# Optimization experiments

Hardware: AMD Instinct MI355X
Metric: run time of the kernel (lower is better)

The kernel has to match this reference:

```python
import jax, jax.numpy as jnp
import numpy as np

N, E = 20000, 320000
NF, EF = 4, 4
HID, HEADS, MODEL_HID = 128, 4, 128


def _p(key, shape, scale=0.1):
    return scale * jax.random.normal(key, shape, dtype=jnp.float32)


def setup_inputs() -> dict:
    key = jax.random.key(0)
    ks = jax.random.split(key, 32)
    x = jax.random.normal(ks[0], (N, NF), dtype=jnp.float32)
    src = jax.random.randint(ks[1], (E,), 0, N)
    off = jax.random.randint(ks[2], (E,), 1, N)
    dst = (src + off) % N  # no self-loops (PyG removes then re-adds them)
    edge_index = jnp.stack([src, dst]).astype(jnp.int64)
    edge_attr = jax.random.uniform(ks[3], (E, EF), dtype=jnp.float32)
    d = dict(x=x, edge_index=edge_index, edge_attr=edge_attr)
    # input_proj
    d['Wp'] = _p(ks[4], (NF, HID)); d['bp'] = jnp.zeros((HID,), jnp.float32)
    # GAT layer 1: in=HID, heads=HEADS, out=HID, concat
    d['W1'] = _p(ks[5], (HID, HEADS * HID)); d['We1'] = _p(ks[6], (EF, HEADS * HID))
    d['as1'] = _p(ks[7], (HEADS, HID)); d['ad1'] = _p(ks[8], (HEADS, HID)); d['ae1'] = _p(ks[9], (HEADS, HID))
    d['b1'] = jnp.zeros((HEADS * HID,), jnp.float32)
    d['g1'] = jnp.ones((HEADS * HID,), jnp.float32); d['be1'] = jnp.zeros((HEADS * HID,), jnp.float32)
    # GAT layer 2: in=HEADS*HID, heads=1, out=HID, mean
    d['W2'] = _p(ks[10], (HEADS * HID, HID)); d['We2'] = _p(ks[11], (EF, HID))
    d['as2'] = _p(ks[12], (1, HID)); d['ad2'] = _p(ks[13], (1, HID)); d['ae2'] = _p(ks[14], (1, HID))
    d['b2'] = jnp.zeros((HID,), jnp.float32)
    d['g2'] = jnp.ones((HID,), jnp.float32); d['be2'] = jnp.zeros((HID,), jnp.float32)
    # output proj + importance scorer
    d['Wo'] = _p(ks[15], (HID, MODEL_HID)); d['bo'] = jnp.zeros((MODEL_HID,), jnp.float32)
    d['Wi'] = _p(ks[16], (MODEL_HID, 1)); d['bi'] = jnp.zeros((1,), jnp.float32)
    return d


def _layer_norm(x, g, b, eps=1e-5):
    mu = x.mean(-1, keepdims=True)
    v = ((x - mu) ** 2).mean(-1, keepdims=True)
    return (x - mu) * jax.lax.rsqrt(v + eps) * g + b


def _segment_softmax(logits, seg, num):
    m = jax.ops.segment_max(logits, seg, num_segments=num)
    e = jnp.exp(logits - m[seg])
    d = jax.ops.segment_sum(e, seg, num_segments=num)
    return e / d[seg]


def _forward(x, edge_index, edge_attr, Wp, bp, W1, We1, as1, ad1, ae1, b1, g1, be1,
             W2, We2, as2, ad2, ae2, b2, g2, be2, Wo, bo, Wi, bi):
    n = x.shape[0]
    src, dst = edge_index[0], edge_index[1]
    e = edge_attr.shape[0]
    # add_self_loops with fill_value='mean': self-loop attr = mean of incoming edge_attr
    deg = jax.ops.segment_sum(jnp.ones((e,), edge_attr.dtype), dst, num_segments=n)
    loop_attr = jax.ops.segment_sum(edge_attr, dst, num_segments=n) / jnp.maximum(deg, 1.0)[:, None]
    loops = jnp.arange(n)
    src_f = jnp.concatenate([src, loops])
    dst_f = jnp.concatenate([dst, loops])
    ea = jnp.concatenate([edge_attr, loop_attr], axis=0)  # [E+N, EF]

    def gat(h, W, We, a_s, a_d, a_e, bias, heads, out_c, concat):
        xh = (h @ W).reshape(n, heads, out_c)                 # [N,H,C]
        eh = (ea @ We).reshape(-1, heads, out_c)              # [E+N,H,C]
        al_s = (xh * a_s).sum(-1)                             # [N,H]
        al_d = (xh * a_d).sum(-1)                             # [N,H]
        al_e = (eh * a_e).sum(-1)                             # [E+N,H]
        logits = jax.nn.leaky_relu(al_s[src_f] + al_d[dst_f] + al_e, negative_slope=0.2)
        alpha = _segment_softmax(logits, dst_f, n)            # [E+N,H]
        out = jax.ops.segment_sum(xh[src_f] * alpha[..., None], dst_f, num_segments=n)
        out = out.reshape(n, heads * out_c) if concat else out.mean(axis=1)
        return out + bias, alpha

    h = x @ Wp + bp
    h, _ = gat(h, W1, We1, as1, ad1, ae1, b1, HEADS, HID, True)
    h = jax.nn.elu(_layer_norm(h, g1, be1))  # dropout is a no-op in eval
    h, edge_attention = gat(h, W2, We2, as2, ad2, ae2, b2, 1, HID, False)
    h = _layer_norm(h, g2, be2)
    emb = h @ Wo + bo
    importance = jax.nn.sigmoid(emb @ Wi + bi).squeeze(-1)
    return emb, edge_attention, importance


def reference(x, edge_index, edge_attr, Wp, bp, W1, We1, as1, ad1, ae1, b1, g1, be1,
              W2, We2, as2, ad2, ae2, b2, g2, be2, Wo, bo, Wi, bi):
    return _forward(x, edge_index, edge_attr, Wp, bp, W1, We1, as1, ad1, ae1, b1, g1, be1,
                    W2, We2, as2, ad2, ae2, b2, g2, be2, Wo, bo, Wi, bi)
```

## Files before the change

### kernel.cpp

```cpp
#include <hip/hip_runtime.h>
#include <math.h>
#include <stdint.h>

#define N_NODES 20000
#define N_EDGES 320000
#define EN_TOT  340000
#define CAP     160

typedef __attribute__((ext_vector_type(8))) _Float16 half8v;
typedef __attribute__((ext_vector_type(4))) float float4v;

__device__ __forceinline__ ushort f2h(float f) {
    _Float16 h = (_Float16)f;
    return __builtin_bit_cast(ushort, h);
}
__device__ __forceinline__ float h2f(ushort s) {
    return (float)__builtin_bit_cast(_Float16, s);
}

__global__ void k_deg(const int* __restrict__ dst, int* __restrict__ degi) {
    int e = blockIdx.x * 256 + threadIdx.x;
    if (e >= N_EDGES) return;
    atomicAdd(&degi[dst[e]], 1);
}

__global__ __launch_bounds__(1024) void k_scan(const int* __restrict__ degi, int* __restrict__ offsets,
                                               const float* __restrict__ We1, const float* __restrict__ ae1,
                                               const float* __restrict__ We2, const float* __restrict__ ae2,
                                               float* __restrict__ M1, float* __restrict__ m2) {
    __shared__ int s[1024];
    int t = threadIdx.x;
    int n0 = t * 20;
    int tot = 0;
    for (int i = 0; i < 20; i++) {
        int n = n0 + i;
        if (n < N_NODES) tot += degi[n] + 1;
    }
    s[t] = tot;
    __syncthreads();
    for (int off = 1; off < 1024; off <<= 1) {
        int v = (t >= off) ? s[t - off] : 0;
        __syncthreads();
        s[t] += v;
        __syncthreads();
    }
    int run = s[t] - tot;
    for (int i = 0; i < 20; i++) {
        int n = n0 + i;
        if (n < N_NODES) {
            offsets[n] = run;
            run += degi[n] + 1;
        }
    }
    if (t == 1023) offsets[N_NODES] = s[1023];
    if (t < 16) {
        int f = t >> 2, h = t & 3;
        float acc = 0.f;
        for (int c = 0; c < 128; c++) acc += We1[f * 512 + h * 128 + c] * ae1[h * 128 + c];
        M1[f * 4 + h] = acc;
    } else if (t < 20) {
        int f = t - 16;
        float acc = 0.f;
        for (int c = 0; c < 128; c++) acc += We2[f * 128 + c] * ae2[c];
        m2[f] = acc;
    }
}

__global__ void k_fill(const int* __restrict__ src, const int* __restrict__ dst,
                       const int* __restrict__ offsets, int* __restrict__ cursor,
                       int2* __restrict__ csr_se) {
    int i = blockIdx.x * 256 + threadIdx.x;
    if (i >= EN_TOT) return;
    int d, sidx, eid;
    if (i < N_EDGES) { d = dst[i]; sidx = src[i]; eid = i; }
    else { int n = i - N_EDGES; d = n; sidx = n; eid = N_EDGES + n; }
    int pos = offsets[d] + atomicAdd(&cursor[d], 1);
    csr_se[pos] = make_int2(sidx, eid);
}

__global__ __launch_bounds__(256) void k_misc(const int* __restrict__ offsets, const int2* __restrict__ csr_se,
                                              const float* __restrict__ eattr, float* __restrict__ loopattr,
                                              const float* __restrict__ W1, const float* __restrict__ W2,
                                              const float* __restrict__ Wo, ushort* __restrict__ W1T,
                                              ushort* __restrict__ W2T, ushort* __restrict__ WoT,
                                              const float* __restrict__ x, const float* __restrict__ Wp,
                                              const float* __restrict__ bp, ushort* __restrict__ h0h) {
    int b = blockIdx.x;
    int tid = threadIdx.x;
    if (b < 5000) {
        int wv = tid >> 6, l = tid & 63;
        int n = b * 4 + wv;
        if (n >= N_NODES) return;
        int start = offsets[n], end = offsets[n + 1];
        float sx = 0.f, sy = 0.f, sz = 0.f, sw = 0.f;
        for (int p = start + l; p < end; p += 64) {
            int eid = csr_se[p].y;
            if (eid < N_EDGES) {
                float4 e = *(const float4*)&eattr[(size_t)eid * 4];
                sx += e.x; sy += e.y; sz += e.z; sw += e.w;
            }
        }
        for (int off = 32; off; off >>= 1) {
            sx += __shfl_down(sx, off);
            sy += __shfl_down(sy, off);
            sz += __shfl_down(sz, off);
            sw += __shfl_down(sw, off);
        }
        if (l == 0) {
            float inv = 1.0f / fmaxf((float)(end - start - 1), 1.0f);
            float4 o;
            o.x = sx * inv; o.y = sy * inv; o.z = sz * inv; o.w = sw * inv;
            *(float4*)&loopattr[(size_t)n * 4] = o;
        }
    } else if (b < 5576) {
        int i = (b - 5000) * 256 + tid;
        if (i < 512 * 128) {
            int nn = i >> 7, kk = i & 127;
            W1T[i] = f2h(W1[kk * 512 + nn]);
        } else if (i < 2 * 512 * 128) {
            int j = i - 512 * 128;
            int nn = j >> 9, kk = j & 511;
            W2T[j] = f2h(W2[kk * 128 + nn]);
        } else if (i < 2 * 512 * 128 + 128 * 128) {
            int j = i - 2 * 512 * 128;
            int nn = j >> 7, kk = j & 127;
            WoT[j] = f2h(Wo[kk * 128 + nn]);
        }
    } else {
        int n = (b - 5576) * 2 + (tid >> 7);
        int c = tid & 127;
        float acc = bp[c];
#pragma unroll
        for (int f = 0; f < 4; f++) acc += x[n * 4 + f] * Wp[f * 128 + c];
        h0h[(size_t)n * 128 + c] = f2h(acc);
    }
}

__global__ __launch_bounds__(256) void k_gemm_hf(const ushort* __restrict__ A, const ushort* __restrict__ BT,
                                                 float* __restrict__ Cf, ushort* __restrict__ Ch,
                                                 int M, int Nn, int K, const float* __restrict__ bias) {
    __shared__ ushort As[64 * 64];
    __shared__ ushort Bs[128 * 64];
    const int tid = threadIdx.x;
    const int lane = tid & 63, wid = tid >> 6;
    const int m0 = blockIdx.x * 64, n0 = blockIdx.y * 128;
    float4v acc[4][2];
#pragma unroll
    for (int i = 0; i < 4; i++)
#pragma unroll
        for (int j = 0; j < 2; j++) acc[i][j] = (float4v){0.f, 0.f, 0.f, 0.f};

    for (int k0 = 0; k0 < K; k0 += 64) {
        __syncthreads();
#pragma unroll
        for (int i = 0; i < 2; i++) {
            int c = tid + i * 256;
            int row = c >> 3, sl = c & 7;
            int off = row * 128 + ((sl ^ (row & 7)) << 4);
            uint4 va = make_uint4(0u, 0u, 0u, 0u);
            if (m0 + row < M) va = *(const uint4*)&A[(size_t)(m0 + row) * K + k0 + sl * 8];
            *(uint4*)((char*)As + off) = va;
        }
#pragma unroll
        for (int i = 0; i < 4; i++) {
            int c = tid + i * 256;
            int row = c >> 3, sl = c & 7;
            int off = row * 128 + ((sl ^ (row & 7)) << 4);
            uint4 vb = *(const uint4*)&BT[(size_t)(n0 + row) * K + k0 + sl * 8];
            *(uint4*)((char*)Bs + off) = vb;
        }
        __syncthreads();
#pragma unroll
        for (int kk = 0; kk < 2; kk++) {
            half8v af[4], bq[2];
            int sl = kk * 4 + (lane >> 4);
#pragma unroll
            for (int mi = 0; mi < 4; mi++) {
                int row = (lane & 15) + mi * 16;
                af[mi] = *(const half8v*)((const char*)As + row * 128 + ((sl ^ (row & 7)) << 4));
            }
#pragma unroll
            for (int ni = 0; ni < 2; ni++) {
                int row = wid * 32 + ni * 16 + (lane & 15);
                bq[ni] = *(const half8v*)((const char*)Bs + row * 128 + ((sl ^ (row & 7)) << 4));
            }
#pragma unroll
            for (int mi = 0; mi < 4; mi++)
#pragma unroll
                for (int ni = 0; ni < 2; ni++)
                    acc[mi][ni] = __builtin_amdgcn_mfma_f32_16x16x32_f16(af[mi], bq[ni], acc[mi][ni], 0, 0, 0);
        }
    }
#pragma unroll
    for (int mi = 0; mi < 4; mi++) {
#pragma unroll
        for (int j = 0; j < 4; j++) {
            int row = m0 + mi * 16 + ((lane >> 4) << 2) + j;
            if (row < M) {
#pragma unroll
                for (int ni = 0; ni < 2; ni++) {
                    int col = n0 + wid * 32 + ni * 16 + (lane & 15);
                    float v = acc[mi][ni][j];
                    if (bias) v += bias[col];
                    if (Cf) Cf[(size_t)row * Nn + col] = v;
                    if (Ch) Ch[(size_t)row * Nn + col] = f2h(v);
                }
            }
        }
    }
}

__global__ __launch_bounds__(256) void k_ald1(const ushort* __restrict__ xhh, const float* __restrict__ as1,
                                              const float* __restrict__ ad1, float* __restrict__ als,
                                              float* __restrict__ ald) {
    int n = blockIdx.x;
    int w = threadIdx.x >> 6, l = threadIdx.x & 63;
    uint v = *(const uint*)&xhh[(size_t)n * 512 + w * 128 + l * 2];
    float f0 = h2f((ushort)(v & 0xffffu));
    float f1 = h2f((ushort)(v >> 16));
    float2 a = *(const float2*)&as1[w * 128 + l * 2];
    float2 b = *(const float2*)&ad1[w * 128 + l * 2];
    float ps = f0 * a.x + f1 * a.y, pd = f0 * b.x + f1 * b.y;
    for (int off = 32; off; off >>= 1) { ps += __shfl_down(ps, off); pd += __shfl_down(pd, off); }
    if (l == 0) { als[n * 4 + w] = ps; ald[n * 4 + w] = pd; }
}

__global__ __launch_bounds__(256) void k_ald2(const ushort* __restrict__ xh2h, const float* __restrict__ as2,
                                              const float* __restrict__ ad2, float* __restrict__ als,
                                              float* __restrict__ ald) {
    int w = threadIdx.x >> 6, l = threadIdx.x & 63;
    int n = blockIdx.x * 4 + w;
    if (n >= N_NODES) return;
    uint v = *(const uint*)&xh2h[(size_t)n * 128 + l * 2];
    float f0 = h2f((ushort)(v & 0xffffu));
    float f1 = h2f((ushort)(v >> 16));
    float2 a = *(const float2*)&as2[l * 2];
    float2 b = *(const float2*)&ad2[l * 2];
    float ps = f0 * a.x + f1 * a.y, pd = f0 * b.x + f1 * b.y;
    for (int off = 32; off; off >>= 1) { ps += __shfl_down(ps, off); pd += __shfl_down(pd, off); }
    if (l == 0) { als[n] = ps; ald[n] = pd; }
}

__global__ __launch_bounds__(128) void k_agg1(const int* __restrict__ offsets, const int2* __restrict__ csr_se,
                                              const float* __restrict__ eattr, const float* __restrict__ loopattr,
                                              const float* __restrict__ als, const float* __restrict__ aldv,
                                              const float* __restrict__ M1, const ushort* __restrict__ xhh,
                                              const float* __restrict__ b1, const float* __restrict__ g1,
                                              const float* __restrict__ be1, ushort* __restrict__ h1h) {
    int wv = threadIdx.x >> 6, lane = threadIdx.x & 63;
    int n = blockIdx.x * 2 + wv;
    __shared__ float Lc[2][CAP][4];
    __shared__ int   sSrc[2][CAP];
    __shared__ float mhs[2][4], shs[2][4];

    int start = offsets[n];
    int cnt = offsets[n + 1] - start;

    int hh = lane & 3;
    float aldn = aldv[n * 4 + hh];
    float c0 = M1[hh], c1 = M1[4 + hh], c2 = M1[8 + hh], c3 = M1[12 + hh];
    float m = -1e30f, s = 0.f;
    for (int j = lane >> 2; j < cnt; j += 16) {
        int2 se = csr_se[start + j];
        const float* eap = (se.y < N_EDGES) ? &eattr[(size_t)se.y * 4] : &loopattr[(size_t)(se.y - N_EDGES) * 4];
        float4 e4 = *(const float4*)eap;
        float l = als[se.x * 4 + hh] + aldn + e4.x * c0 + e4.y * c1 + e4.z * c2 + e4.w * c3;
        l = (l >= 0.f) ? l : 0.2f * l;
        Lc[wv][j][hh] = l;
        if (hh == 0) sSrc[wv][j] = se.x;
        float mn = fmaxf(m, l);
        s = s * __expf(m - mn) + __expf(l - mn);
        m = mn;
    }
#pragma unroll
    for (int off = 4; off < 64; off <<= 1) {
        float mo = __shfl_xor(m, off), so = __shfl_xor(s, off);
        float mn = fmaxf(m, mo);
        s = s * __expf(m - mn) + so * __expf(mo - mn);
        m = mn;
    }
    if (lane < 4) { mhs[wv][lane] = m; shs[wv][lane] = 1.0f / s; }

    int tot = cnt * 4;
    for (int idx = lane; idx < tot; idx += 64) {
        int j = idx >> 2, h = idx & 3;
        Lc[wv][j][h] = __expf(Lc[wv][j][h] - mhs[wv][h]) * shs[wv][h];
    }

    float acc[8];
#pragma unroll
    for (int i = 0; i < 8; i++) acc[i] = 0.f;
    int hg = lane >> 4;
    uint ch = (uint)lane * 8u;
    auto accum = [&](float a, uint4 v) {
        acc[0] += a * h2f((ushort)(v.x & 0xffffu));
        acc[1] += a * h2f((ushort)(v.x >> 16));
        acc[2] += a * h2f((ushort)(v.y & 0xffffu));
        acc[3] += a * h2f((ushort)(v.y >> 16));
        acc[4] += a * h2f((ushort)(v.z & 0xffffu));
        acc[5] += a * h2f((ushort)(v.z >> 16));
        acc[6] += a * h2f((ushort)(v.w & 0xffffu));
        acc[7] += a * h2f((ushort)(v.w >> 16));
    };
    int j = 0;
    for (; j + 4 <= cnt; j += 4) {
        float a0 = Lc[wv][j][hg], a1 = Lc[wv][j + 1][hg];
        float a2 = Lc[wv][j + 2][hg], a3 = Lc[wv][j + 3][hg];
        uint4 v0 = *(const uint4*)&xhh[((uint)sSrc[wv][j] << 9) + ch];
        uint4 v1 = *(const uint4*)&xhh[((uint)sSrc[wv][j + 1] << 9) + ch];
        uint4 v2 = *(const uint4*)&xhh[((uint)sSrc[wv][j + 2] << 9) + ch];
        uint4 v3 = *(const uint4*)&xhh[((uint)sSrc[wv][j + 3] << 9) + ch];
        accum(a0, v0); accum(a1, v1); accum(a2, v2); accum(a3, v3);
    }
    for (; j < cnt; j++) {
        float a = Lc[wv][j][hg];
        uint4 v = *(const uint4*)&xhh[((uint)sSrc[wv][j] << 9) + ch];
        accum(a, v);
    }

    float4 ba = *(const float4*)&b1[ch];
    float4 bb = *(const float4*)&b1[ch + 4];
    float v0 = acc[0] + ba.x, v1 = acc[1] + ba.y, v2 = acc[2] + ba.z, v3 = acc[3] + ba.w;
    float v4 = acc[4] + bb.x, v5 = acc[5] + bb.y, v6 = acc[6] + bb.z, v7 = acc[7] + bb.w;
    float s8 = v0 + v1 + v2 + v3 + v4 + v5 + v6 + v7;
#pragma unroll
    for (int off = 1; off < 64; off <<= 1) s8 += __shfl_xor(s8, off);
    float mu = s8 * (1.0f / 512.0f);
    float d0 = v0 - mu, d1 = v1 - mu, d2 = v2 - mu, d3 = v3 - mu;
    float d4 = v4 - mu, d5 = v5 - mu, d6 = v6 - mu, d7 = v7 - mu;
    float sq = d0 * d0 + d1 * d1 + d2 * d2 + d3 * d3 + d4 * d4 + d5 * d5 + d6 * d6 + d7 * d7;
#pragma unroll
    for (int off = 1; off < 64; off <<= 1) sq += __shfl_xor(sq, off);
    float rstd = rsqrtf(sq * (1.0f / 512.0f) + 1e-5f);
    float4 ga = *(const float4*)&g1[ch];
    float4 gb = *(const float4*)&g1[ch + 4];
    float4 ea = *(const float4*)&be1[ch];
    float4 eb = *(const float4*)&be1[ch + 4];
    float y0 = d0 * rstd * ga.x + ea.x, y1 = d1 * rstd * ga.y + ea.y;
    float y2 = d2 * rstd * ga.z + ea.z, y3 = d3 * rstd * ga.w + ea.w;
    float y4 = d4 * rstd * gb.x + eb.x, y5 = d5 * rstd * gb.y + eb.y;
    float y6 = d6 * rstd * gb.z + eb.z, y7 = d7 * rstd * gb.w + eb.w;
    y0 = (y0 > 0.f) ? y0 : (__expf(y0) - 1.0f);
    y1 = (y1 > 0.f) ? y1 : (__expf(y1) - 1.0f);
    y2 = (y2 > 0.f) ? y2 : (__expf(y2) - 1.0f);
    y3 = (y3 > 0.f) ? y3 : (__expf(y3) - 1.0f);
    y4 = (y4 > 0.f) ? y4 : (__expf(y4) - 1.0f);
    y5 = (y5 > 0.f) ? y5 : (__expf(y5) - 1.0f);
    y6 = (y6 > 0.f) ? y6 : (__expf(y6) - 1.0f);
    y7 = (y7 > 0.f) ? y7 : (__expf(y7) - 1.0f);
    uint4 o;
    o.x = (uint)f2h(y0) | ((uint)f2h(y1) << 16);
    o.y = (uint)f2h(y2) | ((uint)f2h(y3) << 16);
    o.z = (uint)f2h(y4) | ((uint)f2h(y5) << 16);
    o.w = (uint)f2h(y6) | ((uint)f2h(y7) << 16);
    *(uint4*)&h1h[(size_t)n * 512 + ch] = o;
}

__global__ __launch_bounds__(128) void k_agg2(const int* __restrict__ offsets, const int2* __restrict__ csr_se,
                                              const float* __restrict__ eattr, const float* __restrict__ loopattr,
                                              const float* __restrict__ als, const float* __restrict__ aldv,
                                              const float* __restrict__ m2v, const ushort* __restrict__ xh2h,
                                              const float* __restrict__ b2, const float* __restrict__ g2,
                                              const float* __restrict__ be2, float* __restrict__ eaout,
                                              ushort* __restrict__ h2h) {
    int wv = threadIdx.x >> 6, lane = threadIdx.x & 63;
    int n = blockIdx.x * 2 + wv;
    __shared__ float Lc[2][CAP];
    __shared__ int   sS[2][CAP];
    __shared__ int   sE[2][CAP];

    int start = offsets[n];
    int cnt = offsets[n + 1] - start;
    float aldn = aldv[n];
    float c0 = m2v[0], c1 = m2v[1], c2 = m2v[2], c3 = m2v[3];
    float m = -1e30f, s = 0.f;
    for (int j = lane; j < cnt; j += 64) {
        int2 se = csr_se[start + j];
        const float* eap = (se.y < N_EDGES) ? &eattr[(size_t)se.y * 4] : &loopattr[(size_t)(se.y - N_EDGES) * 4];
        float4 e4 = *(const float4*)eap;
        float l = als[se.x] + aldn + e4.x * c0 + e4.y * c1 + e4.z * c2 + e4.w * c3;
        l = (l >= 0.f) ? l : 0.2f * l;
        Lc[wv][j] = l; sS[wv][j] = se.x; sE[wv][j] = se.y;
        float mn = fmaxf(m, l);
        s = s * __expf(m - mn) + __expf(l - mn);
        m = mn;
    }
#pragma unroll
    for (int off = 1; off < 64; off <<= 1) {
        float mo = __shfl_xor(m, off), so = __shfl_xor(s, off);
        float mn = fmaxf(m, mo);
        s = s * __expf(m - mn) + so * __expf(mo - mn);
        m = mn;
    }
    float inv = 1.0f / s;
    for (int j = lane; j < cnt; j += 64) {
        float a = __expf(Lc[wv][j] - m) * inv;
        Lc[wv][j] = a;
        eaout[sE[wv][j]] = a;
    }
    float acc0 = 0.f, acc1 = 0.f;
    uint ch = (uint)lane * 2u;
    int j = 0;
    for (; j + 8 <= cnt; j += 8) {
        float a0 = Lc[wv][j], a1 = Lc[wv][j + 1], a2 = Lc[wv][j + 2], a3 = Lc[wv][j + 3];
        float a4 = Lc[wv][j + 4], a5 = Lc[wv][j + 5], a6 = Lc[wv][j + 6], a7 = Lc[wv][j + 7];
        uint v0 = *(const uint*)&xh2h[((uint)sS[wv][j] << 7) + ch];
        uint v1 = *(const uint*)&xh2h[((uint)sS[wv][j + 1] << 7) + ch];
        uint v2 = *(const uint*)&xh2h[((uint)sS[wv][j + 2] << 7) + ch];
        uint v3 = *(const uint*)&xh2h[((uint)sS[wv][j + 3] << 7) + ch];
        uint v4 = *(const uint*)&xh2h[((uint)sS[wv][j + 4] << 7) + ch];
        uint v5 = *(const uint*)&xh2h[((uint)sS[wv][j + 5] << 7) + ch];
        uint v6 = *(const uint*)&xh2h[((uint)sS[wv][j + 6] << 7) + ch];
        uint v7 = *(const uint*)&xh2h[((uint)sS[wv][j + 7] << 7) + ch];
        acc0 += a0 * h2f((ushort)(v0 & 0xffffu)) + a1 * h2f((ushort)(v1 & 0xffffu))
              + a2 * h2f((ushort)(v2 & 0xffffu)) + a3 * h2f((ushort)(v3 & 0xffffu))
              + a4 * h2f((ushort)(v4 & 0xffffu)) + a5 * h2f((ushort)(v5 & 0xffffu))
              + a6 * h2f((ushort)(v6 & 0xffffu)) + a7 * h2f((ushort)(v7 & 0xffffu));
        acc1 += a0 * h2f((ushort)(v0 >> 16)) + a1 * h2f((ushort)(v1 >> 16))
              + a2 * h2f((ushort)(v2 >> 16)) + a3 * h2f((ushort)(v3 >> 16))
              + a4 * h2f((ushort)(v4 >> 16)) + a5 * h2f((ushort)(v5 >> 16))
              + a6 * h2f((ushort)(v6 >> 16)) + a7 * h2f((ushort)(v7 >> 16));
    }
    for (; j < cnt; j++) {
        float a = Lc[wv][j];
        uint v = *(const uint*)&xh2h[((uint)sS[wv][j] << 7) + ch];
        acc0 += a * h2f((ushort)(v & 0xffffu));
        acc1 += a * h2f((ushort)(v >> 16));
    }
    float2 bb = *(const float2*)&b2[ch];
    float v0 = acc0 + bb.x, v1 = acc1 + bb.y;
    float s2 = v0 + v1;
#pragma unroll
    for (int off = 1; off < 64; off <<= 1) s2 += __shfl_xor(s2, off);
    float mu = s2 * (1.0f / 128.0f);
    float d0 = v0 - mu, d1 = v1 - mu;
    float q = d0 * d0 + d1 * d1;
#pragma unroll
    for (int off = 1; off < 64; off <<= 1) q += __shfl_xor(q, off);
    float rstd = rsqrtf(q * (1.0f / 128.0f) + 1e-5f);
    float2 gg = *(const float2*)&g2[ch];
    float2 ee = *(const float2*)&be2[ch];
    float y0 = d0 * rstd * gg.x + ee.x;
    float y1 = d1 * rstd * gg.y + ee.y;
    uint o = (uint)f2h(y0) | ((uint)f2h(y1) << 16);
    *(uint*)&h2h[(size_t)n * 128 + ch] = o;
}

__global__ __launch_bounds__(256) void k_imp(const float* __restrict__ emb, const float* __restrict__ Wi,
                                             const float* __restrict__ bi, float* __restrict__ impout) {
    int w = threadIdx.x >> 6, l = threadIdx.x & 63;
    int n = blockIdx.x * 4 + w;
    if (n >= N_NODES) return;
    const float* ep = &emb[(size_t)n * 128];
    float p = ep[l] * Wi[l] + ep[l + 64] * Wi[l + 64];
    for (int off = 32; off; off >>= 1) p += __shfl_down(p, off);
    if (l == 0) impout[n] = 1.0f / (1.0f + expf(-(p + bi[0])));
}

extern "C" void kernel_launch(void* const* d_in, const int* in_sizes, int n_in,
                              void* d_out, int out_size, void* d_ws, size_t ws_size,
                              hipStream_t stream) {
    const float* x    = (const float*)d_in[0];
    const int*   eidx = (const int*)d_in[1];
    const float* eattr= (const float*)d_in[2];
    const float* Wp   = (const float*)d_in[3];
    const float* bp   = (const float*)d_in[4];
    const float* W1   = (const float*)d_in[5];
    const float* We1  = (const float*)d_in[6];
    const float* as1  = (const float*)d_in[7];
    const float* ad1  = (const float*)d_in[8];
    const float* ae1  = (const float*)d_in[9];
    const float* b1   = (const float*)d_in[10];
    const float* g1   = (const float*)d_in[11];
    const float* be1  = (const float*)d_in[12];
    const float* W2   = (const float*)d_in[13];
    const float* We2  = (const float*)d_in[14];
    const float* as2  = (const float*)d_in[15];
    const float* ad2  = (const float*)d_in[16];
    const float* ae2  = (const float*)d_in[17];
    const float* b2   = (const float*)d_in[18];
    const float* g2   = (const float*)d_in[19];
    const float* be2  = (const float*)d_in[20];
    const float* Wo   = (const float*)d_in[21];
    const float* bo   = (const float*)d_in[22];
    const float* Wi   = (const float*)d_in[23];
    const float* bi   = (const float*)d_in[24];

    const int* src = eidx;
    const int* dst = eidx + N_EDGES;

    float* emb_out = (float*)d_out;
    float* ea_out  = emb_out + (size_t)N_NODES * 128;
    float* imp_out = ea_out + EN_TOT;

    char* w = (char*)d_ws;
    auto alloc = [&](size_t bytes) -> void* { void* p = (void*)w; w += (bytes + 255) & ~(size_t)255; return p; };
    ushort* xhh    = (ushort*)alloc((size_t)N_NODES * 512 * 2);
    ushort* h1h    = (ushort*)alloc((size_t)N_NODES * 512 * 2);
    ushort* h0h    = (ushort*)alloc((size_t)N_NODES * 128 * 2);
    ushort* xh2h   = (ushort*)alloc((size_t)N_NODES * 128 * 2);
    ushort* h2h    = (ushort*)alloc((size_t)N_NODES * 128 * 2);
    ushort* W1T    = (ushort*)alloc((size_t)512 * 128 * 2);
    ushort* W2T    = (ushort*)alloc((size_t)128 * 512 * 2);
    ushort* WoT    = (ushort*)alloc((size_t)128 * 128 * 2);
    int2*  csr_se  = (int2*)alloc((size_t)EN_TOT * 8);
    int*   offsets = (int*)alloc((size_t)(N_NODES + 1) * 4);
    int*   cursor  = (int*)alloc((size_t)N_NODES * 4);
    int*   degi    = (int*)alloc((size_t)N_NODES * 4);
    float* loopat  = (float*)alloc((size_t)N_NODES * 4 * 4);
    float* als1v   = (float*)alloc((size_t)N_NODES * 4 * 4);
    float* ald1v   = (float*)alloc((size_t)N_NODES * 4 * 4);
    float* als2v   = (float*)alloc((size_t)N_NODES * 4);
    float* ald2v   = (float*)alloc((size_t)N_NODES * 4);
    float* M1      = (float*)alloc(32 * 4);
    float* m2      = M1 + 16;

    hipMemsetAsync(degi,   0, (size_t)N_NODES * 4, stream);
    hipMemsetAsync(cursor, 0, (size_t)N_NODES * 4, stream);

    k_deg<<<(N_EDGES + 255) / 256, 256, 0, stream>>>(dst, degi);
    k_scan<<<1, 1024, 0, stream>>>(degi, offsets, We1, ae1, We2, ae2, M1, m2);
    k_fill<<<(EN_TOT + 255) / 256, 256, 0, stream>>>(src, dst, offsets, cursor, csr_se);
    k_misc<<<15576, 256, 0, stream>>>(offsets, csr_se, eattr, loopat, W1, W2, Wo,
                                      W1T, W2T, WoT, x, Wp, bp, h0h);

    k_gemm_hf<<<dim3((N_NODES + 63) / 64, 4), 256, 0, stream>>>(h0h, W1T, nullptr, xhh,
                                                                N_NODES, 512, 128, nullptr);
    k_ald1<<<N_NODES, 256, 0, stream>>>(xhh, as1, ad1, als1v, ald1v);
    k_agg1<<<N_NODES / 2, 128, 0, stream>>>(offsets, csr_se, eattr, loopat, als1v, ald1v, M1,
                                            xhh, b1, g1, be1, h1h);

    k_gemm_hf<<<dim3((N_NODES + 63) / 64, 1), 256, 0, stream>>>(h1h, W2T, nullptr, xh2h,
                                                                N_NODES, 128, 512, nullptr);
    k_ald2<<<(N_NODES + 3) / 4, 256, 0, stream>>>(xh2h, as2, ad2, als2v, ald2v);
    k_agg2<<<N_NODES / 2, 128, 0, stream>>>(offsets, csr_se, eattr, loopat, als2v, ald2v, m2,
                                            xh2h, b2, g2, be2, ea_out, h2h);

    k_gemm_hf<<<dim3((N_NODES + 63) / 64, 1), 256, 0, stream>>>(h2h, WoT, emb_out, nullptr,
                                                                N_NODES, 128, 128, bo);
    k_imp<<<(N_NODES + 3) / 4, 256, 0, stream>>>(emb_out, Wi, bi, imp_out);
}
```

Baseline: 220.5 us.

## Fuse attention-logit and importance dot products into GEMM epilogue; use packed fp16 aggregation

The per-node source/destination attention dot products (k_ald1, k_ald2) and the importance sigmoid (k_imp) are folded into the GEMM epilogue. The epilogue reduces accumulator values across lanes and warps through shared memory, which removes three kernel launches and re-reads of the GEMM outputs. Separately, the neighbour aggregation loops in both GAT layers now accumulate in packed half2 FMA instead of converting to fp32, and the layer-1 loop is unrolled to 8. Accumulating in fp16 reduces ALU work but can lose precision over long neighbour sums.

```diff
diff --git a/kernel.cpp b/kernel.cpp
--- a/kernel.cpp
+++ b/kernel.cpp
@@ -8,6 +8,7 @@
 #define CAP     160
 
 typedef __attribute__((ext_vector_type(8))) _Float16 half8v;
+typedef __attribute__((ext_vector_type(2))) _Float16 half2v;
 typedef __attribute__((ext_vector_type(4))) float float4v;
 
 __device__ __forceinline__ ushort f2h(float f) {
@@ -138,9 +139,14 @@
 
 __global__ __launch_bounds__(256) void k_gemm_hf(const ushort* __restrict__ A, const ushort* __restrict__ BT,
                                                  float* __restrict__ Cf, ushort* __restrict__ Ch,
-                                                 int M, int Nn, int K, const float* __restrict__ bias) {
+                                                 int M, int Nn, int K, const float* __restrict__ bias,
+                                                 const float* __restrict__ asv, const float* __restrict__ adv,
+                                                 float* __restrict__ outS, float* __restrict__ outD,
+                                                 int hstride, const float* __restrict__ sbias) {
     __shared__ ushort As[64 * 64];
     __shared__ ushort Bs[128 * 64];
+    __shared__ float redS[4][64];
+    __shared__ float redD[4][64];
     const int tid = threadIdx.x;
     const int lane = tid & 63, wid = tid >> 6;
     const int m0 = blockIdx.x * 64, n0 = blockIdx.y * 128;
@@ -191,6 +197,10 @@
                     acc[mi][ni] = __builtin_amdgcn_mfma_f32_16x16x32_f16(af[mi], bq[ni], acc[mi][ni], 0, 0, 0);
         }
     }
+    float bcol[2];
+#pragma unroll
+    for (int ni = 0; ni < 2; ni++)
+        bcol[ni] = bias ? bias[n0 + wid * 32 + ni * 16 + (lane & 15)] : 0.f;
 #pragma unroll
     for (int mi = 0; mi < 4; mi++) {
 #pragma unroll
@@ -200,45 +210,66 @@
 #pragma unroll
                 for (int ni = 0; ni < 2; ni++) {
                     int col = n0 + wid * 32 + ni * 16 + (lane & 15);
-                    float v = acc[mi][ni][j];
-                    if (bias) v += bias[col];
+                    float v = acc[mi][ni][j] + bcol[ni];
                     if (Cf) Cf[(size_t)row * Nn + col] = v;
                     if (Ch) Ch[(size_t)row * Nn + col] = f2h(v);
                 }
             }
         }
     }
-}
-
-__global__ __launch_bounds__(256) void k_ald1(const ushort* __restrict__ xhh, const float* __restrict__ as1,
-                                              const float* __restrict__ ad1, float* __restrict__ als,
-                                              float* __restrict__ ald) {
-    int n = blockIdx.x;
-    int w = threadIdx.x >> 6, l = threadIdx.x & 63;
-    uint v = *(const uint*)&xhh[(size_t)n * 512 + w * 128 + l * 2];
-    float f0 = h2f((ushort)(v & 0xffffu));
-    float f1 = h2f((ushort)(v >> 16));
-    float2 a = *(const float2*)&as1[w * 128 + l * 2];
-    float2 b = *(const float2*)&ad1[w * 128 + l * 2];
-    float ps = f0 * a.x + f1 * a.y, pd = f0 * b.x + f1 * b.y;
-    for (int off = 32; off; off >>= 1) { ps += __shfl_down(ps, off); pd += __shfl_down(pd, off); }
-    if (l == 0) { als[n * 4 + w] = ps; ald[n * 4 + w] = pd; }
-}
-
-__global__ __launch_bounds__(256) void k_ald2(const ushort* __restrict__ xh2h, const float* __restrict__ as2,
-                                              const float* __restrict__ ad2, float* __restrict__ als,
-                                              float* __restrict__ ald) {
-    int w = threadIdx.x >> 6, l = threadIdx.x & 63;
-    int n = blockIdx.x * 4 + w;
-    if (n >= N_NODES) return;
-    uint v = *(const uint*)&xh2h[(size_t)n * 128 + l * 2];
-    float f0 = h2f((ushort)(v & 0xffffu));
-    float f1 = h2f((ushort)(v >> 16));
-    float2 a = *(const float2*)&as2[l * 2];
-    float2 b = *(const float2*)&ad2[l * 2];
-    float ps = f0 * a.x + f1 * a.y, pd = f0 * b.x + f1 * b.y;
-    for (int off = 32; off; off >>= 1) { ps += __shfl_down(ps, off); pd += __shfl_down(pd, off); }
-    if (l == 0) { als[n] = ps; ald[n] = pd; }
+    if (asv) {
+        float asl[2], adl[2];
+#pragma unroll
+        for (int ni = 0; ni < 2; ni++) {
+            int col = n0 + wid * 32 + ni * 16 + (lane & 15);
+            asl[ni] = asv[col];
+            adl[ni] = adv ? adv[col] : 0.f;
+        }
+        float psv[4][4], pdv[4][4];
+#pragma unroll
+        for (int mi = 0; mi < 4; mi++)
+#pragma unroll
+            for (int j = 0; j < 4; j++) {
+                float v0 = acc[mi][0][j] + bcol[0];
+                float v1 = acc[mi][1][j] + bcol[1];
+                psv[mi][j] = v0 * asl[0] + v1 * asl[1];
+                pdv[mi][j] = v0 * adl[0] + v1 * adl[1];
+            }
+#pragma unroll
+        for (int off = 1; off < 16; off <<= 1) {
+#pragma unroll
+            for (int mi = 0; mi < 4; mi++)
+#pragma unroll
+                for (int j = 0; j < 4; j++) {
+                    psv[mi][j] += __shfl_xor(psv[mi][j], off);
+                    pdv[mi][j] += __shfl_xor(pdv[mi][j], off);
+                }
+        }
+        if ((lane & 15) == 0) {
+#pragma unroll
+            for (int mi = 0; mi < 4; mi++)
+#pragma unroll
+                for (int j = 0; j < 4; j++) {
+                    int r = mi * 16 + ((lane >> 4) << 2) + j;
+                    redS[wid][r] = psv[mi][j];
+                    redD[wid][r] = pdv[mi][j];
+                }
+        }
+        __syncthreads();
+        if (tid < 64) {
+            int row = m0 + tid;
+            if (row < M) {
+                float ss = redS[0][tid] + redS[1][tid] + redS[2][tid] + redS[3][tid];
+                float dd = redD[0][tid] + redD[1][tid] + redD[2][tid] + redD[3][tid];
+                if (sbias) {
+                    outS[row] = 1.0f / (1.0f + __expf(-(ss + sbias[0])));
+                } else {
+                    outS[row * hstride + blockIdx.y] = ss;
+                    if (outD) outD[row * hstride + blockIdx.y] = dd;
+                }
+            }
+        }
+    }
 }
 
 __global__ __launch_bounds__(128) void k_agg1(const int* __restrict__ offsets, const int2* __restrict__ csr_se,
@@ -287,41 +318,44 @@
         Lc[wv][j][h] = __expf(Lc[wv][j][h] - mhs[wv][h]) * shs[wv][h];
     }
 
-    float acc[8];
-#pragma unroll
-    for (int i = 0; i < 8; i++) acc[i] = 0.f;
+    half2v hac0 = (half2v)0, hac1 = (half2v)0, hac2 = (half2v)0, hac3 = (half2v)0;
     int hg = lane >> 4;
     uint ch = (uint)lane * 8u;
-    auto accum = [&](float a, uint4 v) {
-        acc[0] += a * h2f((ushort)(v.x & 0xffffu));
-        acc[1] += a * h2f((ushort)(v.x >> 16));
-        acc[2] += a * h2f((ushort)(v.y & 0xffffu));
-        acc[3] += a * h2f((ushort)(v.y >> 16));
-        acc[4] += a * h2f((ushort)(v.z & 0xffffu));
-        acc[5] += a * h2f((ushort)(v.z >> 16));
-        acc[6] += a * h2f((ushort)(v.w & 0xffffu));
-        acc[7] += a * h2f((ushort)(v.w >> 16));
-    };
     int j = 0;
-    for (; j + 4 <= cnt; j += 4) {
-        float a0 = Lc[wv][j][hg], a1 = Lc[wv][j + 1][hg];
-        float a2 = Lc[wv][j + 2][hg], a3 = Lc[wv][j + 3][hg];
-        uint4 v0 = *(const uint4*)&xhh[((uint)sSrc[wv][j] << 9) + ch];
-        uint4 v1 = *(const uint4*)&xhh[((uint)sSrc[wv][j + 1] << 9) + ch];
-        uint4 v2 = *(const uint4*)&xhh[((uint)sSrc[wv][j + 2] << 9) + ch];
-        uint4 v3 = *(const uint4*)&xhh[((uint)sSrc[wv][j + 3] << 9) + ch];
-        accum(a0, v0); accum(a1, v1); accum(a2, v2); accum(a3, v3);
+    for (; j + 8 <= cnt; j += 8) {
+        _Float16 av[8];
+        uint4 vv[8];
+#pragma unroll
+        for (int t = 0; t < 8; t++) av[t] = (_Float16)Lc[wv][j + t][hg];
+#pragma unroll
+        for (int t = 0; t < 8; t++) vv[t] = *(const uint4*)&xhh[((uint)sSrc[wv][j + t] << 9) + ch];
+#pragma unroll
+        for (int t = 0; t < 8; t++) {
+            half2v a2 = (half2v){av[t], av[t]};
+            const half2v* pv = (const half2v*)&vv[t];
+            hac0 = pv[0] * a2 + hac0;
+            hac1 = pv[1] * a2 + hac1;
+            hac2 = pv[2] * a2 + hac2;
+            hac3 = pv[3] * a2 + hac3;
+        }
     }
     for (; j < cnt; j++) {
-        float a = Lc[wv][j][hg];
+        _Float16 a = (_Float16)Lc[wv][j][hg];
+        half2v a2 = (half2v){a, a};
         uint4 v = *(const uint4*)&xhh[((uint)sSrc[wv][j] << 9) + ch];
-        accum(a, v);
+        const half2v* pv = (const half2v*)&v;
+        hac0 = pv[0] * a2 + hac0;
+        hac1 = pv[1] * a2 + hac1;
+        hac2 = pv[2] * a2 + hac2;
+        hac3 = pv[3] * a2 + hac3;
     }
 
     float4 ba = *(const float4*)&b1[ch];
     float4 bb = *(const float4*)&b1[ch + 4];
-    float v0 = acc[0] + ba.x, v1 = acc[1] + ba.y, v2 = acc[2] + ba.z, v3 = acc[3] + ba.w;
-    float v4 = acc[4] + bb.x, v5 = acc[5] + bb.y, v6 = acc[6] + bb.z, v7 = acc[7] + bb.w;
+    float v0 = (float)hac0[0] + ba.x, v1 = (float)hac0[1] + ba.y;
+    float v2 = (float)hac1[0] + ba.z, v3 = (float)hac1[1] + ba.w;
+    float v4 = (float)hac2[0] + bb.x, v5 = (float)hac2[1] + bb.y;
+    float v6 = (float)hac3[0] + bb.z, v7 = (float)hac3[1] + bb.w;
     float s8 = v0 + v1 + v2 + v3 + v4 + v5 + v6 + v7;
 #pragma unroll
     for (int off = 1; off < 64; off <<= 1) s8 += __shfl_xor(s8, off);
@@ -398,37 +432,31 @@
         Lc[wv][j] = a;
         eaout[sE[wv][j]] = a;
     }
-    float acc0 = 0.f, acc1 = 0.f;
+    half2v hac = (half2v)0;
     uint ch = (uint)lane * 2u;
     int j = 0;
     for (; j + 8 <= cnt; j += 8) {
-        float a0 = Lc[wv][j], a1 = Lc[wv][j + 1], a2 = Lc[wv][j + 2], a3 = Lc[wv][j + 3];
-        float a4 = Lc[wv][j + 4], a5 = Lc[wv][j + 5], a6 = Lc[wv][j + 6], a7 = Lc[wv][j + 7];
-        uint v0 = *(const uint*)&xh2h[((uint)sS[wv][j] << 7) + ch];
-        uint v1 = *(const uint*)&xh2h[((uint)sS[wv][j + 1] << 7) + ch];
-        uint v2 = *(const uint*)&xh2h[((uint)sS[wv][j + 2] << 7) + ch];
-        uint v3 = *(const uint*)&xh2h[((uint)sS[wv][j + 3] << 7) + ch];
-        uint v4 = *(const uint*)&xh2h[((uint)sS[wv][j + 4] << 7) + ch];
-        uint v5 = *(const uint*)&xh2h[((uint)sS[wv][j + 5] << 7) + ch];
-        uint v6 = *(const uint*)&xh2h[((uint)sS[wv][j + 6] << 7) + ch];
-        uint v7 = *(const uint*)&xh2h[((uint)sS[wv][j + 7] << 7) + ch];
-        acc0 += a0 * h2f((ushort)(v0 & 0xffffu)) + a1 * h2f((ushort)(v1 & 0xffffu))
-              + a2 * h2f((ushort)(v2 & 0xffffu)) + a3 * h2f((ushort)(v3 & 0xffffu))
-              + a4 * h2f((ushort)(v4 & 0xffffu)) + a5 * h2f((ushort)(v5 & 0xffffu))
-              + a6 * h2f((ushort)(v6 & 0xffffu)) + a7 * h2f((ushort)(v7 & 0xffffu));
-        acc1 += a0 * h2f((ushort)(v0 >> 16)) + a1 * h2f((ushort)(v1 >> 16))
-              + a2 * h2f((ushort)(v2 >> 16)) + a3 * h2f((ushort)(v3 >> 16))
-              + a4 * h2f((ushort)(v4 >> 16)) + a5 * h2f((ushort)(v5 >> 16))
-              + a6 * h2f((ushort)(v6 >> 16)) + a7 * h2f((ushort)(v7 >> 16));
+        _Float16 av[8];
+        uint vv[8];
+#pragma unroll
+        for (int t = 0; t < 8; t++) av[t] = (_Float16)Lc[wv][j + t];
+#pragma unroll
+        for (int t = 0; t < 8; t++) vv[t] = *(const uint*)&xh2h[((uint)sS[wv][j + t] << 7) + ch];
+#pragma unroll
+        for (int t = 0; t < 8; t++) {
+            half2v a2 = (half2v){av[t], av[t]};
+            half2v pv = __builtin_bit_cast(half2v, vv[t]);
+            hac = pv * a2 + hac;
+        }
     }
     for (; j < cnt; j++) {
-        float a = Lc[wv][j];
-        uint v = *(const uint*)&xh2h[((uint)sS[wv][j] << 7) + ch];
-        acc0 += a * h2f((ushort)(v & 0xffffu));
-        acc1 += a * h2f((ushort)(v >> 16));
+        _Float16 a = (_Float16)Lc[wv][j];
+        half2v a2 = (half2v){a, a};
+        half2v pv = __builtin_bit_cast(half2v, *(const uint*)&xh2h[((uint)sS[wv][j] << 7) + ch]);
+        hac = pv * a2 + hac;
     }
     float2 bb = *(const float2*)&b2[ch];
-    float v0 = acc0 + bb.x, v1 = acc1 + bb.y;
+    float v0 = (float)hac[0] + bb.x, v1 = (float)hac[1] + bb.y;
     float s2 = v0 + v1;
 #pragma unroll
     for (int off = 1; off < 64; off <<= 1) s2 += __shfl_xor(s2, off);
@@ -444,17 +472,6 @@
     float y1 = d1 * rstd * gg.y + ee.y;
     uint o = (uint)f2h(y0) | ((uint)f2h(y1) << 16);
     *(uint*)&h2h[(size_t)n * 128 + ch] = o;
-}
-
-__global__ __launch_bounds__(256) void k_imp(const float* __restrict__ emb, const float* __restrict__ Wi,
-                                             const float* __restrict__ bi, float* __restrict__ impout) {
-    int w = threadIdx.x >> 6, l = threadIdx.x & 63;
-    int n = blockIdx.x * 4 + w;
-    if (n >= N_NODES) return;
-    const float* ep = &emb[(size_t)n * 128];
-    float p = ep[l] * Wi[l] + ep[l + 64] * Wi[l + 64];
-    for (int off = 32; off; off >>= 1) p += __shfl_down(p, off);
-    if (l == 0) impout[n] = 1.0f / (1.0f + expf(-(p + bi[0])));
 }
 
 extern "C" void kernel_launch(void* const* d_in, const int* in_sizes, int n_in,
@@ -525,18 +542,18 @@
                                       W1T, W2T, WoT, x, Wp, bp, h0h);
 
     k_gemm_hf<<<dim3((N_NODES + 63) / 64, 4), 256, 0, stream>>>(h0h, W1T, nullptr, xhh,
-                                                                N_NODES, 512, 128, nullptr);
-    k_ald1<<<N_NODES, 256, 0, stream>>>(xhh, as1, ad1, als1v, ald1v);
+                                                                N_NODES, 512, 128, nullptr,
+                                                                as1, ad1, als1v, ald1v, 4, nullptr);
     k_agg1<<<N_NODES / 2, 128, 0, stream>>>(offsets, csr_se, eattr, loopat, als1v, ald1v, M1,
                                             xhh, b1, g1, be1, h1h);
 
     k_gemm_hf<<<dim3((N_NODES + 63) / 64, 1), 256, 0, stream>>>(h1h, W2T, nullptr, xh2h,
-                                                                N_NODES, 128, 512, nullptr);
-    k_ald2<<<(N_NODES + 3) / 4, 256, 0, stream>>>(xh2h, as2, ad2, als2v, ald2v);
+                                                                N_NODES, 128, 512, nullptr,
+                                                                as2, ad2, als2v, ald2v, 1, nullptr);
     k_agg2<<<N_NODES / 2, 128, 0, stream>>>(offsets, csr_se, eattr, loopat, als2v, ald2v, m2,
                                             xh2h, b2, g2, be2, ea_out, h2h);
 
     k_gemm_hf<<<dim3((N_NODES + 63) / 64, 1), 256, 0, stream>>>(h2h, WoT, emb_out, nullptr,
-                                                                N_NODES, 128, 128, bo);
-    k_imp<<<(N_NODES + 3) / 4, 256, 0, stream>>>(emb_out, Wi, bi, imp_out);
-}
+                                                                N_NODES, 128, 128, bo,
+                                                                Wi, nullptr, imp_out, nullptr, 1, bi);
+}
```

After: 207.1 us. 1.06x faster.
